# Optimization experiments

Hardware: AMD Instinct MI355X
Metric: run time of the kernel (lower is better)

Reference implementation:

```python
import jax, jax.numpy as jnp
import numpy as np

B, T, F_IN, F_OUT, N, TP, K = 32, 12, 16, 32, 2048, 12, 3
RED = 4  # SE reduction ratio


def _conv2d(x, w, b):
    # x: [b,c,h,w_] NCHW, w: [o,i,kh,kw] OIHW, VALID padding (matches nn.Conv2d default)
    y = jax.lax.conv_general_dilated(x, w, window_strides=(1, 1), padding='VALID',
                                     dimension_numbers=('NCHW', 'OIHW', 'NCHW'))
    return y + b[None, :, None, None]


def _tconv(x, w, b, tp):
    # Tconv1: conv (1,2) -> self-pad time axis back to tp with trailing slices -> relu
    y = _conv2d(x, w, b)
    t = y.shape[-1]
    if t < tp:
        y = jnp.concatenate([y[..., -(tp - t):], y], axis=-1)
    return jax.nn.relu(y)


def setup_inputs() -> dict:
    rng = np.random.default_rng(0)
    # symmetric nonneg adjacency
    W = rng.random((N, N), dtype=np.float32)
    W = (W + W.T) * 0.5
    D = np.diag(W.sum(axis=1))
    L = (D - W).astype(np.float32)
    # lambda_max via power iteration (replaces scipy eigs 'LR')
    v = rng.standard_normal(N).astype(np.float32)
    for _ in range(100):
        v = L @ v
        v /= np.linalg.norm(v)
    lam = float(v @ (L @ v))
    Lt = (2.0 * L / lam - np.eye(N, dtype=np.float32)).astype(np.float32)
    # NOTE: original code uses ELEMENTWISE '*' (numpy) in the Chebyshev recurrence; replicate faithfully
    cheb = [np.eye(N, dtype=np.float32), Lt.copy()]
    for _ in range(2, K):
        cheb.append(2.0 * Lt * cheb[-1] - cheb[-2])
    cheb = jnp.asarray(np.stack(cheb))  # [K, N, N]

    key = jax.random.key(0)
    ks = jax.random.split(key, 16)
    s = 0.05
    hid = T // RED
    return {
        'x': jax.random.normal(ks[0], (B, T, F_IN, N), dtype=jnp.float32),
        'cheb': cheb,
        'theta1': jax.random.normal(ks[1], (K, F_IN, F_OUT), dtype=jnp.float32) * s,
        'theta2': jax.random.normal(ks[2], (K, F_OUT, F_OUT), dtype=jnp.float32) * s,
        'mlp1_w': jax.random.normal(ks[3], (hid, T), dtype=jnp.float32) * s,
        'mlp1_b': jnp.zeros((hid,), dtype=jnp.float32),
        'mlp2_w': jax.random.normal(ks[4], (T, hid), dtype=jnp.float32) * s,
        'mlp2_b': jnp.zeros((T,), dtype=jnp.float32),
        'tc1_w': jax.random.normal(ks[5], (F_OUT, F_OUT, 1, 2), dtype=jnp.float32) * s,
        'tc1_b': jnp.zeros((F_OUT,), dtype=jnp.float32),
        'tc2_w': jax.random.normal(ks[6], (F_OUT, F_OUT, 1, 2), dtype=jnp.float32) * s,
        'tc2_b': jnp.zeros((F_OUT,), dtype=jnp.float32),
        'res_w': jax.random.normal(ks[7], (F_OUT, F_IN, 1, 1), dtype=jnp.float32) * s,
        'res_b': jnp.zeros((F_OUT,), dtype=jnp.float32),
        'ln_g': jnp.ones((N,), dtype=jnp.float32),
        'ln_b': jnp.zeros((N,), dtype=jnp.float32),
    }


def reference(x, cheb, theta1, theta2, mlp1_w, mlp1_b, mlp2_w, mlp2_b,
              tc1_w, tc1_b, tc2_w, tc2_b, res_w, res_b, ln_g, ln_b):
    # --- SE channel attention over the t axis ---
    att = x.mean(axis=(2, 3))                            # [b,t] (AvgPool over full (f,n))
    att = jax.nn.relu(att @ mlp1_w.T + mlp1_b)
    att = jax.nn.sigmoid(att @ mlp2_w.T + mlp2_b)
    x_att = x * att[:, :, None, None]                    # [b,t,f,n]

    # --- Chebyshev graph conv: fused over time t and order k ---
    def gconv(h, theta):
        # original: for t, for k: (h[b,:,f,t] @ T_k) then (@ theta_k), summed over k
        z = jnp.einsum('btfm,kmn->bktfn', h, cheb)       # graph mixing, [b,K,t,f,n]
        return jnp.einsum('bktfn,kfo->bton', z, theta)   # feature mixing + k-sum -> [b,t,o,n]

    xg = jax.nn.relu(gconv(x_att, theta1))
    xg = jax.nn.relu(gconv(xg, theta2))                  # [b,t,F_OUT,n]

    # --- temporal convs ---
    xt = _tconv(xg.transpose(0, 2, 3, 1), tc1_w, tc1_b, TP)   # [b,F_OUT,n,TP]
    xt = _tconv(xt, tc2_w, tc2_b, TP).transpose(0, 3, 1, 2)   # [b,TP,F_OUT,n]

    # --- residual 1x1 conv on the original input ---
    tshort = xg.shape[1] - xt.shape[1]                   # == 0 with t == tp
    x_res = _conv2d(x[:, tshort:].transpose(0, 2, 3, 1), res_w, res_b).transpose(0, 3, 1, 2)

    y = xt + x_res                                       # [b,TP,F_OUT,n]
    # LayerNorm over last (node) axis, eps=1e-5, biased variance (torch default)
    mu = y.mean(axis=-1, keepdims=True)
    var = ((y - mu) ** 2).mean(axis=-1, keepdims=True)
    y = (y - mu) / jnp.sqrt(var + 1e-5) * ln_g + ln_b
    return jax.nn.relu(y)
```

## Files before the change

kernel.cpp:

```cpp
#include <hip/hip_runtime.h>

#define DI __device__ __forceinline__

typedef __attribute__((ext_vector_type(8))) short short8;
typedef __attribute__((ext_vector_type(4))) float f32x4;

static constexpr int Bb  = 32;
static constexpr int Tt  = 12;
static constexpr int FIN = 16;
static constexpr int NN  = 2048;
static constexpr int HID = 3;
static constexpr int M1  = Bb*Tt*FIN;
static constexpr int M2  = Bb*Tt*32;

DI float b2f(unsigned short u){
  unsigned int v = ((unsigned int)u) << 16;
  float f; __builtin_memcpy(&f, &v, 4); return f;
}
DI unsigned short f2b(float f){
  unsigned int v; __builtin_memcpy(&v, &f, 4);
  v = v + 0x7FFFu + ((v >> 16) & 1u);
  return (unsigned short)(v >> 16);
}
DI float ld(const void* p, size_t i, int flag){
  return flag ? b2f(((const unsigned short*)p)[i]) : ((const float*)p)[i];
}

typedef __attribute__((address_space(1))) const unsigned int g_u32;
typedef __attribute__((address_space(3))) unsigned int l_u32;
DI void gll16(const unsigned short* g, unsigned short* l){
  __builtin_amdgcn_global_load_lds((g_u32*)g, (l_u32*)l, 16, 0, 0);
}

__global__ void k_sniff(const unsigned short* __restrict__ x, int* __restrict__ flag){
  int tid = threadIdx.x;
  float v = b2f(x[tid*2]);
  int bad = (!(v == v)) || (fabsf(v) > 1e6f);
  unsigned long long m = __ballot(bad);
  if (tid == 0) *flag = (m == 0ull) ? 1 : 0;
}

__global__ void k_convert(const void* __restrict__ src, unsigned short* __restrict__ dst,
                          long long n8, const int* __restrict__ flagp, long long off){
  int flag = *flagp;
  long long i = (long long)blockIdx.x*256 + threadIdx.x;
  if (i >= n8) return;
  size_t base = (size_t)i * 8;
  if (flag){
    *(uint4*)(dst + base) = *(const uint4*)((const unsigned short*)src + off + base);
  } else {
    const float* f = (const float*)src + off + base;
    unsigned short o[8];
    #pragma unroll
    for (int j = 0; j < 8; ++j) o[j] = f2b(f[j]);
    uint4 ov; __builtin_memcpy(&ov, o, 16);
    *(uint4*)(dst + base) = ov;
  }
}

__global__ void k_att_mean(const void* __restrict__ x, float* __restrict__ att0,
                           const int* __restrict__ flagp){
  int flag = *flagp;
  int bt = blockIdx.x; int tid = threadIdx.x;
  size_t base = (size_t)bt * FIN * NN;
  float s = 0.f;
  for (int i = tid; i < FIN*NN; i += 256) s += ld(x, base + i, flag);
  for (int off = 32; off; off >>= 1) s += __shfl_down(s, off);
  __shared__ float red[4];
  if ((tid & 63) == 0) red[tid >> 6] = s;
  __syncthreads();
  if (tid == 0) att0[bt] = (red[0]+red[1]+red[2]+red[3]) * (1.f / (FIN*NN));
}

__global__ void k_att_mlp(const float* __restrict__ att0,
                          const void* __restrict__ m1w, const void* __restrict__ m1b,
                          const void* __restrict__ m2w, const void* __restrict__ m2b,
                          float* __restrict__ att, const int* __restrict__ flagp){
  int flag = *flagp;
  int b = threadIdx.x;
  if (b >= Bb) return;
  float a[Tt];
  #pragma unroll
  for (int t = 0; t < Tt; ++t) a[t] = att0[b*Tt + t];
  float h[HID];
  #pragma unroll
  for (int j = 0; j < HID; ++j){
    float s = ld(m1b, j, flag);
    #pragma unroll
    for (int t = 0; t < Tt; ++t) s += a[t] * ld(m1w, j*Tt + t, flag);
    h[j] = s > 0.f ? s : 0.f;
  }
  #pragma unroll
  for (int t = 0; t < Tt; ++t){
    float s = ld(m2b, t, flag);
    #pragma unroll
    for (int j = 0; j < HID; ++j) s += h[j] * ld(m2w, t*HID + j, flag);
    att[b*Tt + t] = 1.f / (1.f + expf(-s));
  }
}

DI void stage_tile(const unsigned short* __restrict__ Ag,
                   const unsigned short* __restrict__ chb,
                   unsigned short* Ad, unsigned short* Bd,
                   int row0, int gn0, int kk0, int tid){
  #pragma unroll
  for (int p = 0; p < 2; ++p){
    int s = tid + p*256, r = s >> 2, j = s & 3;
    gll16(Ag + (size_t)(row0 + r)*NN + kk0 + ((j ^ (r & 3)) << 3), Ad + (s << 3));
  }
  #pragma unroll
  for (int p = 0; p < 4; ++p){
    int s = tid + p*256, k = s >> 9, rem = s & 511, r = rem >> 2, j = rem & 3;
    gll16(chb + (size_t)k*NN*NN + (size_t)(gn0 + r)*NN + kk0 + ((j ^ (r & 3)) << 3), Bd + (s << 3));
  }
}

DI void compute_tile(const unsigned short* As, const unsigned short* Bs,
                     f32x4 (&acc)[2][8][2], int w, int cc, int q){
  short8 af[8];
  #pragma unroll
  for (int mt = 0; mt < 8; ++mt)
    af[mt] = *(const short8*)(As + ((mt*16 + cc) << 5) + ((q ^ (cc & 3)) << 3));
  #pragma unroll
  for (int k = 0; k < 2; ++k){
    #pragma unroll
    for (int ns = 0; ns < 2; ++ns){
      int r = w*32 + ns*16 + cc;
      short8 bv = *(const short8*)(Bs + (((k << 7) + r) << 5) + ((q ^ (cc & 3)) << 3));
      #pragma unroll
      for (int mt = 0; mt < 8; ++mt)
        acc[k][mt][ns] = __builtin_amdgcn_mfma_f32_16x16x32_bf16(af[mt], bv, acc[k][mt][ns], 0, 0, 0);
    }
  }
}

template <int SCALE, int F>
__global__ __launch_bounds__(256, 2)
void k_gemm(const unsigned short* __restrict__ Ag,
            const float* __restrict__ att,
            const unsigned short* __restrict__ chb,
            const void* __restrict__ theta,
            unsigned short* __restrict__ X,
            const int* __restrict__ flagp){
  constexpr int Kp = (F == 16) ? 64 : 96;
  constexpr int PP = (F == 16) ? 72 : 104;
  constexpr int G  = 128 / F;
  constexpr int NKB = Kp / 32;
  constexpr int BUF = 128*32 + 2*128*32;

  __shared__ __align__(16) unsigned short SMEM[2*BUF];
  __shared__ __align__(16) unsigned short TT[32*PP];

  int flag = *flagp;
  int tid  = threadIdx.x;
  int w    = tid >> 6, lane = tid & 63, q = lane >> 4, cc = lane & 15;
  int row0 = blockIdx.x * 128;
  int gn0  = blockIdx.y * 128;

  for (int idx = tid; idx < 32*PP; idx += 256){
    int o = idx / PP, kk = idx % PP;
    float v = (kk < 3*F) ? ld(theta, (size_t)kk*32 + o, flag) : 0.f;
    TT[idx] = f2b(v);
  }

  unsigned short* A0 = SMEM;
  unsigned short* B0 = SMEM + 4096;
  unsigned short* A1 = SMEM + BUF;
  unsigned short* B1 = SMEM + BUF + 4096;

  f32x4 zero4 = {0.f, 0.f, 0.f, 0.f};
  f32x4 acc[2][8][2];
  #pragma unroll
  for (int k = 0; k < 2; ++k)
    #pragma unroll
    for (int mt = 0; mt < 8; ++mt)
      #pragma unroll
      for (int ns = 0; ns < 2; ++ns) acc[k][mt][ns] = zero4;

  stage_tile(Ag, chb, A0, B0, row0, gn0, 0, tid);
  __syncthreads();

  for (int it = 0; it < 62; it += 2){
    stage_tile(Ag, chb, A1, B1, row0, gn0, (it+1)*32, tid);
    compute_tile(A0, B0, acc, w, cc, q);
    __syncthreads();
    stage_tile(Ag, chb, A0, B0, row0, gn0, (it+2)*32, tid);
    compute_tile(A1, B1, acc, w, cc, q);
    __syncthreads();
  }
  stage_tile(Ag, chb, A1, B1, row0, gn0, 63*32, tid);
  compute_tile(A0, B0, acc, w, cc, q);
  __syncthreads();
  compute_tile(A1, B1, acc, w, cc, q);
  __syncthreads();

  unsigned short* zs = SMEM + w * (32*PP);

  short8 afm[2][NKB];
  #pragma unroll
  for (int mt_o = 0; mt_o < 2; ++mt_o)
    #pragma unroll
    for (int kb = 0; kb < NKB; ++kb)
      afm[mt_o][kb] = *(const short8*)(TT + (mt_o*16 + cc)*PP + kb*32 + q*8);

  if (F == 16){
    if (lane < 32){
      #pragma unroll
      for (int j = 0; j < 4; ++j) *(uint2*)(zs + lane*PP + 48 + j*4) = make_uint2(0u, 0u);
    }
  }

  int bt0 = row0 / F;
  #pragma unroll
  for (int g = 0; g < G; ++g){
    float sc = SCALE ? att[bt0 + g] : 1.f;
    #pragma unroll
    for (int pass = 0; pass < F/16; ++pass){
      int rf = pass*16 + (lane >> 2), c8 = (lane & 3) * 8;
      uint4 u = *(const uint4*)(Ag + (size_t)(row0 + g*F + rf)*NN + gn0 + w*32 + c8);
      unsigned short sp[8]; __builtin_memcpy(sp, &u, 16);
      #pragma unroll
      for (int e = 0; e < 8; ++e){
        unsigned short val = SCALE ? f2b(b2f(sp[e]) * sc) : sp[e];
        zs[(c8 + e)*PP + rf] = val;
      }
    }
    #pragma unroll
    for (int k = 0; k < 2; ++k)
      #pragma unroll
      for (int mt_l = 0; mt_l < F/16; ++mt_l)
        #pragma unroll
        for (int ns = 0; ns < 2; ++ns){
          int mt = g*(F/16) + mt_l;
          f32x4 v = acc[k][mt][ns];
          #pragma unroll
          for (int r = 0; r < 4; ++r){
            float pv = SCALE ? v[r] * sc : v[r];
            zs[(ns*16 + cc)*PP + F*(k+1) + mt_l*16 + q*4 + r] = f2b(pv);
          }
        }
    #pragma unroll
    for (int mt_o = 0; mt_o < 2; ++mt_o)
      #pragma unroll
      for (int ch = 0; ch < 2; ++ch){
        f32x4 am = zero4;
        #pragma unroll
        for (int kb = 0; kb < NKB; ++kb){
          short8 bm = *(const short8*)(zs + (ch*16 + cc)*PP + kb*32 + q*8);
          am = __builtin_amdgcn_mfma_f32_16x16x32_bf16(afm[mt_o][kb], bm, am, 0, 0, 0);
        }
        #pragma unroll
        for (int r = 0; r < 4; ++r){
          int o = mt_o*16 + q*4 + r;
          float v = am[r]; v = v > 0.f ? v : 0.f;
          X[((size_t)((bt0 + g)*32 + o))*NN + gn0 + w*32 + ch*16 + cc] = f2b(v);
        }
      }
  }
}

__global__ void k_tconv1(const unsigned short* __restrict__ xin,
                         const void* __restrict__ wgt, const void* __restrict__ bias,
                         unsigned short* __restrict__ yout, const int* __restrict__ flagp){
  int flag = *flagp;
  __shared__ float wl[32*32*2];
  __shared__ float bl[32];
  int tid = threadIdx.x;
  for (int i = tid; i < 2048; i += 256) wl[i] = ld(wgt, i, flag);
  if (tid < 32) bl[tid] = ld(bias, tid, flag);
  __syncthreads();
  int bt = blockIdx.x, b = bt / 12, t = bt % 12;
  int c = (t == 0) ? 10 : (t - 1);
  int n = blockIdx.y*256 + tid;
  const unsigned short* p0 = xin + ((size_t)(b*12 + c  )*32)*NN + n;
  const unsigned short* p1 = xin + ((size_t)(b*12 + c+1)*32)*NN + n;
  float acc[32];
  #pragma unroll
  for (int o = 0; o < 32; ++o) acc[o] = bl[o];
  for (int i = 0; i < 32; ++i){
    float v0 = b2f(p0[(size_t)i*NN]);
    float v1 = b2f(p1[(size_t)i*NN]);
    #pragma unroll
    for (int o = 0; o < 32; ++o) acc[o] += v0*wl[o*64 + i*2] + v1*wl[o*64 + i*2 + 1];
  }
  unsigned short* op = yout + ((size_t)bt*32)*NN + n;
  #pragma unroll
  for (int o = 0; o < 32; ++o){ float v = acc[o]; op[(size_t)o*NN] = f2b(v > 0.f ? v : 0.f); }
}

__global__ void k_tail(const unsigned short* __restrict__ yp,
                       const void* __restrict__ x,
                       const void* __restrict__ w2, const void* __restrict__ b2v,
                       const void* __restrict__ rw, const void* __restrict__ rbv,
                       const void* __restrict__ lng, const void* __restrict__ lnb,
                       void* __restrict__ out, const int* __restrict__ flagp){
  int flag = *flagp;
  __shared__ float wl[8*32*2];
  __shared__ float rl[8*16];
  __shared__ float bcv[8], rbc[8];
  __shared__ float redS[4*8], redS2[4*8];
  int tid = threadIdx.x;
  int bt = blockIdx.x, og = blockIdx.y, o0 = og*8;
  int b = bt / 12, t = bt % 12, c = (t == 0) ? 10 : (t - 1);
  for (int i = tid; i < 512; i += 256){ int oo = i >> 6, rem = i & 63; wl[i] = ld(w2, (o0 + oo)*64 + rem, flag); }
  for (int i = tid; i < 128; i += 256){ int oo = i >> 4, ii = i & 15; rl[i] = ld(rw, (o0 + oo)*16 + ii, flag); }
  if (tid < 8){ bcv[tid] = ld(b2v, o0 + tid, flag); rbc[tid] = ld(rbv, o0 + tid, flag); }
  __syncthreads();
  float acc[8][8];
  #pragma unroll
  for (int oo = 0; oo < 8; ++oo)
    #pragma unroll
    for (int nn = 0; nn < 8; ++nn) acc[oo][nn] = bcv[oo];
  const unsigned short* p0 = yp + ((size_t)(b*12 + c  )*32)*NN;
  const unsigned short* p1 = yp + ((size_t)(b*12 + c+1)*32)*NN;
  for (int i = 0; i < 32; ++i){
    float v0[8], v1[8];
    #pragma unroll
    for (int nn = 0; nn < 8; ++nn){
      int n = nn*256 + tid;
      v0[nn] = b2f(p0[(size_t)i*NN + n]);
      v1[nn] = b2f(p1[(size_t)i*NN + n]);
    }
    #pragma unroll
    for (int oo = 0; oo < 8; ++oo){
      float w0 = wl[oo*64 + i*2], w1 = wl[oo*64 + i*2 + 1];
      #pragma unroll
      for (int nn = 0; nn < 8; ++nn) acc[oo][nn] += v0[nn]*w0 + v1[nn]*w1;
    }
  }
  #pragma unroll
  for (int oo = 0; oo < 8; ++oo)
    #pragma unroll
    for (int nn = 0; nn < 8; ++nn){ float v = acc[oo][nn]; acc[oo][nn] = (v > 0.f ? v : 0.f) + rbc[oo]; }
  size_t xbase = ((size_t)(b*12 + t)*16)*NN;
  for (int i = 0; i < 16; ++i){
    float xv[8];
    #pragma unroll
    for (int nn = 0; nn < 8; ++nn) xv[nn] = ld(x, xbase + (size_t)i*NN + nn*256 + tid, flag);
    #pragma unroll
    for (int oo = 0; oo < 8; ++oo){
      float r = rl[oo*16 + i];
      #pragma unroll
      for (int nn = 0; nn < 8; ++nn) acc[oo][nn] += xv[nn]*r;
    }
  }
  int lane = tid & 63, wv = tid >> 6;
  #pragma unroll
  for (int oo = 0; oo < 8; ++oo){
    float s = 0.f, s2 = 0.f;
    #pragma unroll
    for (int nn = 0; nn < 8; ++nn){ float v = acc[oo][nn]; s += v; s2 += v*v; }
    for (int off = 32; off; off >>= 1){ s += __shfl_down(s, off); s2 += __shfl_down(s2, off); }
    if (lane == 0){ redS[wv*8 + oo] = s; redS2[wv*8 + oo] = s2; }
  }
  __syncthreads();
  float mu[8], inv[8];
  #pragma unroll
  for (int oo = 0; oo < 8; ++oo){
    float S  = redS [oo] + redS [8 + oo] + redS [16 + oo] + redS [24 + oo];
    float S2 = redS2[oo] + redS2[8 + oo] + redS2[16 + oo] + redS2[24 + oo];
    float m = S * (1.f/2048.f);
    float var = S2 * (1.f/2048.f) - m*m;
    mu[oo] = m; inv[oo] = rsqrtf(var + 1e-5f);
  }
  size_t obase = ((size_t)((b*12 + t)*32 + o0))*NN;
  #pragma unroll
  for (int nn = 0; nn < 8; ++nn){
    int n = nn*256 + tid;
    float g = ld(lng, n, flag), be = ld(lnb, n, flag);
    #pragma unroll
    for (int oo = 0; oo < 8; ++oo){
      float v = (acc[oo][nn] - mu[oo])*inv[oo]*g + be;
      v = v > 0.f ? v : 0.f;
      if (flag) ((unsigned short*)out)[obase + (size_t)oo*NN + n] = f2b(v);
      else      ((float*)out)[obase + (size_t)oo*NN + n] = v;
    }
  }
}

extern "C" void kernel_launch(void* const* d_in, const int* in_sizes, int n_in,
                              void* d_out, int out_size, void* d_ws, size_t ws_size,
                              hipStream_t stream){
  const void* x    = d_in[0];
  const void* cheb = d_in[1];
  const void* th1  = d_in[2];
  const void* th2  = d_in[3];
  const void* m1w  = d_in[4];
  const void* m1b  = d_in[5];
  const void* m2w  = d_in[6];
  const void* m2b  = d_in[7];
  const void* t1w  = d_in[8];
  const void* t1b  = d_in[9];
  const void* t2w  = d_in[10];
  const void* t2b  = d_in[11];
  const void* rw   = d_in[12];
  const void* rb   = d_in[13];
  const void* lng  = d_in[14];
  const void* lnb  = d_in[15];
  char* ws = (char*)d_ws;

  int*   flag  = (int*)ws;
  float* att0  = (float*)(ws + 4096);
  float* att   = (float*)(ws + 8192);
  unsigned short* xb  = (unsigned short*)(ws + 16384);
  unsigned short* chb = xb + (size_t)M1*NN;
  unsigned short* X1  = chb + (size_t)2*NN*NN;
  unsigned short* X2  = (unsigned short*)d_out;
  unsigned short* Y1  = X1;

  k_sniff  <<<1, 64, 0, stream>>>((const unsigned short*)x, flag);
  k_convert<<<((long long)M1*NN/8 + 255)/256, 256, 0, stream>>>(x, xb, (long long)M1*NN/8, flag, 0);
  k_convert<<<((long long)2*NN*NN/8 + 255)/256, 256, 0, stream>>>(cheb, chb, (long long)2*NN*NN/8, flag, (long long)NN*NN);
  k_att_mean<<<384, 256, 0, stream>>>(x, att0, flag);
  k_att_mlp <<<1, 64, 0, stream>>>(att0, m1w, m1b, m2w, m2b, att, flag);

  k_gemm<1,16><<<dim3(M1/128, 16), 256, 0, stream>>>(xb, att, chb, th1, X1, flag);
  k_gemm<0,32><<<dim3(M2/128, 16), 256, 0, stream>>>(X1, att, chb, th2, X2, flag);

  k_tconv1<<<dim3(384, 8), 256, 0, stream>>>(X2, t1w, t1b, Y1, flag);
  k_tail  <<<dim3(384, 4), 256, 0, stream>>>(Y1, x, t2w, t2b, rw, rb, lng, lnb, d_out, flag);
}
```

Baseline: 782.9 us.

## Triple-buffer GEMM LDS staging with vmcnt waits and swizzle block order

Replaces the double-buffered main loop with a three-stage LDS ring. Each iteration issues the load two tiles ahead and waits with partial vmcnt counts and raw s_barrier instead of a full __syncthreads, so global loads can overlap more compute. The block index is also remapped with an 8-way swizzle to change the order in which tiles are scheduled, aiming for better L2 reuse. LDS use grows by half, which may cut occupancy below the 2-blocks target. The hardcoded vmcnt values assume stage_tile issues exactly 6 loads per tile.

```diff
diff --git a/kernel.cpp b/kernel.cpp
--- a/kernel.cpp
+++ b/kernel.cpp
@@ -30,6 +30,12 @@
 typedef __attribute__((address_space(3))) unsigned int l_u32;
 DI void gll16(const unsigned short* g, unsigned short* l){
   __builtin_amdgcn_global_load_lds((g_u32*)g, (l_u32*)l, 16, 0, 0);
+}
+
+DI void bar(){
+  asm volatile("" ::: "memory");
+  __builtin_amdgcn_s_barrier();
+  asm volatile("" ::: "memory");
 }
 
 __global__ void k_sniff(const unsigned short* __restrict__ x, int* __restrict__ flag){
@@ -132,6 +138,12 @@
         acc[k][mt][ns] = __builtin_amdgcn_mfma_f32_16x16x32_bf16(af[mt], bv, acc[k][mt][ns], 0, 0, 0);
     }
   }
+}
+
+DI void phase_end(){
+  asm volatile("s_waitcnt lgkmcnt(0)" ::: "memory");
+  __builtin_amdgcn_sched_barrier(0);
+  bar();
 }
 
 template <int SCALE, int F>
@@ -148,14 +160,19 @@
   constexpr int NKB = Kp / 32;
   constexpr int BUF = 128*32 + 2*128*32;
 
-  __shared__ __align__(16) unsigned short SMEM[2*BUF];
+  __shared__ __align__(16) unsigned short SMEM[3*BUF];
   __shared__ __align__(16) unsigned short TT[32*PP];
 
   int flag = *flagp;
   int tid  = threadIdx.x;
   int w    = tid >> 6, lane = tid & 63, q = lane >> 4, cc = lane & 15;
-  int row0 = blockIdx.x * 128;
-  int gn0  = blockIdx.y * 128;
+
+  int nbx  = gridDim.x;
+  int flat = blockIdx.y * nbx + blockIdx.x;
+  int chunk = (nbx * (int)gridDim.y) >> 3;
+  int swz  = (flat & 7) * chunk + (flat >> 3);
+  int row0 = (swz % nbx) * 128;
+  int gn0  = (swz / nbx) * 128;
 
   for (int idx = tid; idx < 32*PP; idx += 256){
     int o = idx / PP, kk = idx % PP;
@@ -163,11 +180,6 @@
     TT[idx] = f2b(v);
   }
 
-  unsigned short* A0 = SMEM;
-  unsigned short* B0 = SMEM + 4096;
-  unsigned short* A1 = SMEM + BUF;
-  unsigned short* B1 = SMEM + BUF + 4096;
-
   f32x4 zero4 = {0.f, 0.f, 0.f, 0.f};
   f32x4 acc[2][8][2];
   #pragma unroll
@@ -177,21 +189,32 @@
       #pragma unroll
       for (int ns = 0; ns < 2; ++ns) acc[k][mt][ns] = zero4;
 
-  stage_tile(Ag, chb, A0, B0, row0, gn0, 0, tid);
-  __syncthreads();
-
-  for (int it = 0; it < 62; it += 2){
-    stage_tile(Ag, chb, A1, B1, row0, gn0, (it+1)*32, tid);
-    compute_tile(A0, B0, acc, w, cc, q);
-    __syncthreads();
-    stage_tile(Ag, chb, A0, B0, row0, gn0, (it+2)*32, tid);
-    compute_tile(A1, B1, acc, w, cc, q);
-    __syncthreads();
-  }
-  stage_tile(Ag, chb, A1, B1, row0, gn0, 63*32, tid);
-  compute_tile(A0, B0, acc, w, cc, q);
-  __syncthreads();
-  compute_tile(A1, B1, acc, w, cc, q);
+  unsigned short *Ac = SMEM,           *Bc = SMEM + 4096;
+  unsigned short *An = SMEM +   BUF,   *Bn = SMEM +   BUF + 4096;
+  unsigned short *Aq = SMEM + 2*BUF,   *Bq = SMEM + 2*BUF + 4096;
+
+  stage_tile(Ag, chb, Ac, Bc, row0, gn0, 0,  tid);
+  stage_tile(Ag, chb, An, Bn, row0, gn0, 32, tid);
+
+  for (int it = 0; it < 62; ++it){
+    stage_tile(Ag, chb, Aq, Bq, row0, gn0, (it + 2) * 32, tid);
+    asm volatile("s_waitcnt vmcnt(12)" ::: "memory");
+    bar();
+    compute_tile(Ac, Bc, acc, w, cc, q);
+    phase_end();
+    unsigned short* t0 = Ac; Ac = An; An = Aq; Aq = t0;
+    unsigned short* t1 = Bc; Bc = Bn; Bn = Bq; Bq = t1;
+  }
+  asm volatile("s_waitcnt vmcnt(6)" ::: "memory");
+  bar();
+  compute_tile(Ac, Bc, acc, w, cc, q);
+  phase_end();
+  { unsigned short* t0 = Ac; Ac = An; An = Aq; Aq = t0;
+    unsigned short* t1 = Bc; Bc = Bn; Bn = Bq; Bq = t1; }
+  asm volatile("s_waitcnt vmcnt(0)" ::: "memory");
+  bar();
+  compute_tile(Ac, Bc, acc, w, cc, q);
+
   __syncthreads();
 
   unsigned short* zs = SMEM + w * (32*PP);
```

Result: slower. 837.0 us (+6.9%).
